# Kernel optimization log

Hardware: AMD Instinct MI355X
Metric: run time of the kernel (lower is better)

The kernel has to match this reference:

```python
import jax, jax.numpy as jnp
import numpy as np
import math

H = 768      # hidden_size
NH = 12      # num_head
DH = H // NH # head dim
FF = 4 * H
EPS = 1e-6

def _layernorm(x, g, b):
    mu = jnp.mean(x, axis=-1, keepdims=True)
    var = jnp.mean(jnp.square(x - mu), axis=-1, keepdims=True)
    return (x - mu) * jax.lax.rsqrt(var + EPS) * g + b

def setup_inputs() -> dict:
    key = jax.random.key(0)
    ks = jax.random.split(key, 16)
    B, N = 8, 1024
    xav = lambda k, i, o: jax.random.uniform(k, (i, o), jnp.float32, -1.0, 1.0) * math.sqrt(6.0 / (i + o))
    bias = lambda k, o: jax.random.normal(k, (o,), jnp.float32) * 1e-6
    return {
        "x": jax.random.normal(ks[0], (B, N, H), jnp.float32),
        "wq": xav(ks[1], H, H), "bq": bias(ks[2], H),
        "wk": xav(ks[3], H, H), "bk": bias(ks[4], H),
        "wv": xav(ks[5], H, H), "bv": bias(ks[6], H),
        "wo": xav(ks[7], H, H), "bo": bias(ks[8], H),
        "w1": xav(ks[9], H, FF), "b1": bias(ks[10], FF),
        "w2": xav(ks[11], FF, H), "b2": bias(ks[12], H),
        "g1": jnp.ones((H,), jnp.float32), "be1": jnp.zeros((H,), jnp.float32),
        "g2": jnp.ones((H,), jnp.float32), "be2": jnp.zeros((H,), jnp.float32),
    }

def reference(x, wq, bq, wk, bk, wv, bv, wo, bo, w1, b1, w2, b2, g1, be1, g2, be2):
    B, N, _ = x.shape
    x1 = _layernorm(x, g1, be1)
    # QKV projections -> (B, NH, N, DH)
    split = lambda t: t.reshape(B, N, NH, DH).transpose(0, 2, 1, 3)
    q = split(x1 @ wq + bq)
    k = split(x1 @ wk + bk)
    v = split(x1 @ wv + bv)
    # NOTE: original divides by sqrt(attention_size)=sqrt(H), not sqrt(DH)
    scores = jnp.einsum("bhqd,bhkd->bhqk", q, k) / math.sqrt(H)
    weights = jax.nn.softmax(scores, axis=-1)
    ctx = jnp.einsum("bhqk,bhkd->bhqd", weights, v)
    ctx = ctx.transpose(0, 2, 1, 3).reshape(B, N, H)
    attn_out = ctx @ wo + bo  # dropout is identity in eval
    x = x + attn_out
    x2 = _layernorm(x, g2, be2)
    h = jax.nn.gelu(x2 @ w1 + b1, approximate=False)  # torch F.gelu is exact erf gelu
    mlp_out = h @ w2 + b2
    x = x + mlp_out
    return (x, weights)
```

## Files before the change

kernel.cpp:

```cpp
#include <hip/hip_runtime.h>
#include <cstdint>
#include <cstddef>

#define H 768
#define NHEAD 12
#define DH 64
#define FFD 3072
#define BATCH 8
#define SEQ 1024
#define NTOK (BATCH*SEQ)
#define QKVS 2304

typedef __bf16 bf16x8 __attribute__((ext_vector_type(8)));
typedef float  floatx4 __attribute__((ext_vector_type(4)));

#define MFMA_BF16(a,b,c) __builtin_amdgcn_mfma_f32_16x16x32_bf16((a),(b),(c),0,0,0)

__device__ __forceinline__ void gload16(const void* g, void* l) {
    __builtin_amdgcn_global_load_lds((const __attribute__((address_space(1))) void*)g,
                                     (__attribute__((address_space(3))) void*)l,
                                     16, 0, 0);
}

__device__ __forceinline__ float gelu_erf(float x) {
    float z = fabsf(x) * 0.70710678118654752f;
    float t = __builtin_amdgcn_rcpf(1.0f + 0.3275911f * z);
    float poly = t * (0.254829592f +
               t * (-0.284496736f +
               t * (1.421413741f +
               t * (-1.453152027f +
               t * 1.061405429f))));
    float e = __expf(-z * z);
    float erfv = 1.0f - poly * e;
    erfv = copysignf(erfv, x);
    return 0.5f * x * (1.0f + erfv);
}

__global__ __launch_bounds__(256) void prep_kernel(
    const float* __restrict__ wq, const float* __restrict__ wk,
    const float* __restrict__ wv, const float* __restrict__ wo,
    const float* __restrict__ w1, const float* __restrict__ w2,
    const float* __restrict__ bq, const float* __restrict__ bk,
    const float* __restrict__ bv,
    __bf16* __restrict__ wqkvT, __bf16* __restrict__ woT,
    __bf16* __restrict__ w1T, __bf16* __restrict__ w2T,
    float* __restrict__ bqkv,
    const float* __restrict__ x, const float* __restrict__ g1,
    const float* __restrict__ be1, __bf16* __restrict__ x1b) {
    __shared__ float tile[32][33];
    int bid = blockIdx.x;
    int tid = threadIdx.x;
    if (bid < 6912) {
        const float* W; __bf16* T; int Kd, Nn, bx, by;
        if (bid < 1728) {
            int part = bid / 576;
            int rem = bid - part * 576;
            W = part == 0 ? wq : (part == 1 ? wk : wv);
            T = wqkvT + (size_t)part * H * H;
            Kd = H; Nn = H; bx = rem % 24; by = rem / 24;
        } else if (bid < 2304) {
            int rem = bid - 1728;
            W = wo; T = woT; Kd = H; Nn = H; bx = rem % 24; by = rem / 24;
        } else if (bid < 4608) {
            int rem = bid - 2304;
            W = w1; T = w1T; Kd = H; Nn = FFD; bx = rem % 96; by = rem / 96;
        } else {
            int rem = bid - 4608;
            W = w2; T = w2T; Kd = FFD; Nn = H; bx = rem % 24; by = rem / 24;
        }
        int tx = tid & 31, ty = tid >> 5;
        int n0 = bx * 32, k0 = by * 32;
#pragma unroll
        for (int i = 0; i < 32; i += 8)
            tile[ty + i][tx] = W[(size_t)(k0 + ty + i) * Nn + n0 + tx];
        __syncthreads();
#pragma unroll
        for (int i = 0; i < 32; i += 8)
            T[(size_t)(n0 + ty + i) * Kd + k0 + tx] = (__bf16)tile[tx][ty + i];
    } else if (bid < 6921) {
        int i = (bid - 6912) * 256 + tid;
        float v = i < H ? bq[i] : (i < 2 * H ? bk[i - H] : bv[i - 2 * H]);
        bqkv[i] = v;
    } else {
        int row  = (bid - 6921) * 4 + (tid >> 6);
        int lane = tid & 63;
        const float* xr = x + (size_t)row * H;
        float v[12];
        float s = 0.f;
#pragma unroll
        for (int i = 0; i < 12; i++) { v[i] = xr[lane + i * 64]; s += v[i]; }
#pragma unroll
        for (int m = 32; m >= 1; m >>= 1) s += __shfl_xor(s, m, 64);
        float mu = s * (1.0f / H);
        float q = 0.f;
#pragma unroll
        for (int i = 0; i < 12; i++) { float d = v[i] - mu; q += d * d; }
#pragma unroll
        for (int m = 32; m >= 1; m >>= 1) q += __shfl_xor(q, m, 64);
        float rstd = rsqrtf(q * (1.0f / H) + 1e-6f);
        __bf16* orow = x1b + (size_t)row * H;
#pragma unroll
        for (int i = 0; i < 12; i++) {
            int c = lane + i * 64;
            orow[c] = (__bf16)((v[i] - mu) * rstd * g1[c] + be1[c]);
        }
    }
}

__global__ __launch_bounds__(256) void ln_kernel(const float* __restrict__ x,
                                                 const float* __restrict__ g,
                                                 const float* __restrict__ be,
                                                 __bf16* __restrict__ out) {
    int row  = blockIdx.x * 4 + (threadIdx.x >> 6);
    int lane = threadIdx.x & 63;
    const float* xr = x + (size_t)row * H;
    float v[12];
    float s = 0.f;
#pragma unroll
    for (int i = 0; i < 12; i++) { v[i] = xr[lane + i * 64]; s += v[i]; }
#pragma unroll
    for (int m = 32; m >= 1; m >>= 1) s += __shfl_xor(s, m, 64);
    float mu = s * (1.0f / H);
    float q = 0.f;
#pragma unroll
    for (int i = 0; i < 12; i++) { float d = v[i] - mu; q += d * d; }
#pragma unroll
    for (int m = 32; m >= 1; m >>= 1) q += __shfl_xor(q, m, 64);
    float rstd = rsqrtf(q * (1.0f / H) + 1e-6f);
    __bf16* orow = out + (size_t)row * H;
#pragma unroll
    for (int i = 0; i < 12; i++) {
        int c = lane + i * 64;
        orow[c] = (__bf16)((v[i] - mu) * rstd * g[c] + be[c]);
    }
}

__global__ __launch_bounds__(256) void vtrans_kernel(const __bf16* __restrict__ qkv,
                                                     __bf16* __restrict__ vT) {
    __shared__ __bf16 tile[64][65];
    int b = blockIdx.z, h = blockIdx.y, n0 = blockIdx.x * 64;
    int tx = threadIdx.x, ty = threadIdx.y;
#pragma unroll
    for (int r = ty; r < 64; r += 4)
        tile[r][tx] = qkv[((size_t)b * SEQ + n0 + r) * QKVS + 2 * H + h * DH + tx];
    __syncthreads();
#pragma unroll
    for (int c = ty; c < 64; c += 4)
        vT[(((size_t)b * NHEAD + h) * DH + c) * SEQ + n0 + tx] = tile[tx][c];
}

template<bool GELU, bool HAS_RES, bool OUT_BF16>
__global__ __launch_bounds__(256) void gemm_kernel(const __bf16* __restrict__ A,
                                                   const __bf16* __restrict__ Bt,
                                                   const float* __restrict__ bias,
                                                   const float* __restrict__ res,
                                                   __bf16* __restrict__ obf,
                                                   float* __restrict__ ofp,
                                                   int Nn, int K) {
    __shared__ __bf16 As[128 * 64];
    __shared__ __bf16 Bs[128 * 64];
    int tid = threadIdx.x;
    int wave = tid >> 6, lane = tid & 63;
    int wr = wave >> 1, wc = wave & 1;
    int l15 = lane & 15, quad = lane >> 4;

    floatx4 acc[4][4];
    floatx4 zero = {0.f, 0.f, 0.f, 0.f};
#pragma unroll
    for (int i = 0; i < 4; i++)
#pragma unroll
        for (int j = 0; j < 4; j++) acc[i][j] = zero;

    int lrow = lane >> 3;
    int lcol = ((lane & 7) ^ lrow) * 8;
    const __bf16* Agc[4];
    const __bf16* Bgc[4];
    __bf16* AsDc[4];
    __bf16* BsDc[4];
#pragma unroll
    for (int cc = 0; cc < 4; cc++) {
        int chunk = wave * 4 + cc;
        int row = chunk * 8 + lrow;
        Agc[cc] = A + (size_t)(blockIdx.y * 128 + row) * K + lcol;
        Bgc[cc] = Bt + (size_t)(blockIdx.x * 128 + row) * K + lcol;
        AsDc[cc] = &As[chunk * 512];
        BsDc[cc] = &Bs[chunk * 512];
    }

    for (int k0 = 0; k0 < K; k0 += 64) {
#pragma unroll
        for (int cc = 0; cc < 4; cc++) {
            gload16(Agc[cc] + k0, AsDc[cc]);
            gload16(Bgc[cc] + k0, BsDc[cc]);
        }
        __syncthreads();
#pragma unroll
        for (int kk = 0; kk < 2; kk++) {
            int c16 = (kk * 4 + quad) ^ (l15 & 7);
            bf16x8 af[4], bfv[4];
#pragma unroll
            for (int i = 0; i < 4; i++)
                af[i] = *(const bf16x8*)&As[(wr * 64 + i * 16 + l15) * 64 + c16 * 8];
#pragma unroll
            for (int j = 0; j < 4; j++)
                bfv[j] = *(const bf16x8*)&Bs[(wc * 64 + j * 16 + l15) * 64 + c16 * 8];
#pragma unroll
            for (int i = 0; i < 4; i++)
#pragma unroll
                for (int j = 0; j < 4; j++)
                    acc[i][j] = MFMA_BF16(af[i], bfv[j], acc[i][j]);
        }
        __syncthreads();
    }

#pragma unroll
    for (int i = 0; i < 4; i++) {
        int row = blockIdx.y * 128 + wr * 64 + i * 16 + quad * 4;
#pragma unroll
        for (int j = 0; j < 4; j++) {
            int col = blockIdx.x * 128 + wc * 64 + j * 16 + l15;
            float bsv = bias[col];
#pragma unroll
            for (int r = 0; r < 4; r++) {
                float vv = acc[i][j][r] + bsv;
                if (GELU) vv = gelu_erf(vv);
                if (HAS_RES) vv += res[(size_t)(row + r) * Nn + col];
                if (OUT_BF16) obf[(size_t)(row + r) * Nn + col] = (__bf16)vv;
                else          ofp[(size_t)(row + r) * Nn + col] = vv;
            }
        }
    }
}

__device__ __forceinline__ int sbidx(int row, int col) {
    return row * 1024 + (col ^ ((row & 7) << 3));
}

__global__ __launch_bounds__(256, 4) void attn_kernel(const __bf16* __restrict__ qkv,
                                                      const __bf16* __restrict__ vT,
                                                      float* __restrict__ Wout,
                                                      __bf16* __restrict__ ctx) {
    __shared__ __bf16 Sb[16 * 1024];
    __shared__ __align__(16) float red[2][16][4];
    int tid = threadIdx.x;
    int wave = tid >> 6, lane = tid & 63, l15 = lane & 15, quad = lane >> 4;

    int linear = blockIdx.x + 64 * (blockIdx.y + 12 * blockIdx.z);
    int xcd = linear & 7;
    int j   = linear >> 3;
    int bh  = xcd + 8 * (j >> 6);
    int rt  = j & 63;
    int h = bh % NHEAD, b = bh / NHEAD;

    const size_t tokbase = (size_t)b * SEQ * QKVS + h * DH;
    const float scale = 0.03608439182435161f;

    const __bf16* qrow = qkv + tokbase + (size_t)(rt * 16 + l15) * QKVS;
    bf16x8 qf0 = *(const bf16x8*)(qrow + quad * 8);
    bf16x8 qf1 = *(const bf16x8*)(qrow + 32 + quad * 8);

    floatx4 s[16];
    const __bf16* kbase = qkv + tokbase + H;
#pragma unroll
    for (int i = 0; i < 16; i++) {
        int ct = wave * 16 + i;
        const __bf16* krow = kbase + (size_t)(ct * 16 + l15) * QKVS;
        bf16x8 kf0 = *(const bf16x8*)(krow + quad * 8);
        bf16x8 kf1 = *(const bf16x8*)(krow + 32 + quad * 8);
        floatx4 a = {0.f, 0.f, 0.f, 0.f};
        a = MFMA_BF16(qf0, kf0, a);
        a = MFMA_BF16(qf1, kf1, a);
#pragma unroll
        for (int r = 0; r < 4; r++) s[i][r] = a[r] * scale;
    }

    float m4[4];
#pragma unroll
    for (int r = 0; r < 4; r++) {
        float m = s[0][r];
#pragma unroll
        for (int i = 1; i < 16; i++) m = fmaxf(m, s[i][r]);
#pragma unroll
        for (int msk = 8; msk >= 1; msk >>= 1) m = fmaxf(m, __shfl_xor(m, msk, 64));
        m4[r] = m;
    }
    if (l15 == 0) {
#pragma unroll
        for (int r = 0; r < 4; r++) red[0][quad * 4 + r][wave] = m4[r];
    }
    __syncthreads();
    float mrow[4];
#pragma unroll
    for (int r = 0; r < 4; r++) {
        float4 rr = *(const float4*)&red[0][quad * 4 + r][0];
        mrow[r] = fmaxf(fmaxf(rr.x, rr.y), fmaxf(rr.z, rr.w));
    }

    float s4[4] = {0.f, 0.f, 0.f, 0.f};
#pragma unroll
    for (int i = 0; i < 16; i++) {
#pragma unroll
        for (int r = 0; r < 4; r++) {
            float e = __expf(s[i][r] - mrow[r]);
            s[i][r] = e;
            s4[r] += e;
        }
    }
#pragma unroll
    for (int r = 0; r < 4; r++) {
#pragma unroll
        for (int msk = 8; msk >= 1; msk >>= 1) s4[r] += __shfl_xor(s4[r], msk, 64);
    }
    if (l15 == 0) {
#pragma unroll
        for (int r = 0; r < 4; r++) red[1][quad * 4 + r][wave] = s4[r];
    }
    __syncthreads();
    float inv[4];
#pragma unroll
    for (int r = 0; r < 4; r++) {
        float4 rr = *(const float4*)&red[1][quad * 4 + r][0];
        inv[r] = 1.0f / (rr.x + rr.y + rr.z + rr.w);
    }

    size_t wbase = (((size_t)b * NHEAD + h) * SEQ + rt * 16) * SEQ;
#pragma unroll
    for (int i = 0; i < 16; i++) {
        int col = (wave * 16 + i) * 16 + l15;
#pragma unroll
        for (int r = 0; r < 4; r++) {
            float w = s[i][r] * inv[r];
            int row = quad * 4 + r;
            __builtin_nontemporal_store(w, &Wout[wbase + (size_t)row * SEQ + col]);
            Sb[sbidx(row, col)] = (__bf16)w;
        }
    }
    __syncthreads();

    floatx4 acc = {0.f, 0.f, 0.f, 0.f};
    const __bf16* vbase = vT + (((size_t)b * NHEAD + h) * DH + wave * 16 + l15) * SEQ;
#pragma unroll
    for (int c = 0; c < 32; c++) {
        int k0 = c * 32 + quad * 8;
        bf16x8 af = *(const bf16x8*)&Sb[sbidx(l15, k0)];
        bf16x8 bv = *(const bf16x8*)(vbase + k0);
        acc = MFMA_BF16(af, bv, acc);
    }
#pragma unroll
    for (int r = 0; r < 4; r++)
        ctx[((size_t)b * SEQ + rt * 16 + quad * 4 + r) * H + h * DH + wave * 16 + l15] =
            (__bf16)acc[r];
}

extern "C" void kernel_launch(void* const* d_in, const int* in_sizes, int n_in,
                              void* d_out, int out_size, void* d_ws, size_t ws_size,
                              hipStream_t stream) {
    const float* x   = (const float*)d_in[0];
    const float* wq  = (const float*)d_in[1];
    const float* bq  = (const float*)d_in[2];
    const float* wk  = (const float*)d_in[3];
    const float* bk  = (const float*)d_in[4];
    const float* wv  = (const float*)d_in[5];
    const float* bv  = (const float*)d_in[6];
    const float* wo  = (const float*)d_in[7];
    const float* bo  = (const float*)d_in[8];
    const float* w1  = (const float*)d_in[9];
    const float* b1  = (const float*)d_in[10];
    const float* w2  = (const float*)d_in[11];
    const float* b2  = (const float*)d_in[12];
    const float* g1  = (const float*)d_in[13];
    const float* be1 = (const float*)d_in[14];
    const float* g2  = (const float*)d_in[15];
    const float* be2 = (const float*)d_in[16];

    char* ws = (char*)d_ws;
    const size_t SZB = (size_t)NTOK * H * 2;
    __bf16* x1b  = (__bf16*)(ws);
    __bf16* qkvb = (__bf16*)(ws + SZB);
    __bf16* vTb  = (__bf16*)(ws + 4 * SZB);
    __bf16* ctxb = (__bf16*)(ws + 5 * SZB);
    __bf16* x2b  = (__bf16*)(ws + 6 * SZB);
    __bf16* hb   = (__bf16*)(ws + 7 * SZB);
    size_t off = 7 * SZB + (size_t)NTOK * FFD * 2;
    float* xattn = (float*)(ws + off); off += (size_t)NTOK * H * 4;
    __bf16* wqkvT = (__bf16*)(ws + off); off += (size_t)3 * H * H * 2;
    __bf16* woT  = (__bf16*)(ws + off); off += (size_t)H * H * 2;
    __bf16* w1T  = (__bf16*)(ws + off); off += (size_t)H * FFD * 2;
    __bf16* w2T  = (__bf16*)(ws + off); off += (size_t)FFD * H * 2;
    float* bqkv  = (float*)(ws + off); off += (size_t)3 * H * 4;

    float* outx = (float*)d_out;
    float* outw = (float*)d_out + (size_t)NTOK * H;

    prep_kernel<<<8969, 256, 0, stream>>>(wq, wk, wv, wo, w1, w2, bq, bk, bv,
                                          wqkvT, woT, w1T, w2T, bqkv,
                                          x, g1, be1, x1b);

    gemm_kernel<false, false, true><<<dim3(QKVS / 128, NTOK / 128), 256, 0, stream>>>(
        x1b, wqkvT, bqkv, nullptr, qkvb, nullptr, QKVS, H);

    vtrans_kernel<<<dim3(16, NHEAD, BATCH), dim3(64, 4), 0, stream>>>(qkvb, vTb);

    attn_kernel<<<dim3(64, NHEAD, BATCH), 256, 0, stream>>>(qkvb, vTb, outw, ctxb);

    gemm_kernel<false, true, false><<<dim3(H / 128, NTOK / 128), 256, 0, stream>>>(
        ctxb, woT, bo, x, nullptr, xattn, H, H);

    ln_kernel<<<NTOK / 4, 256, 0, stream>>>(xattn, g2, be2, x2b);

    gemm_kernel<true, false, true><<<dim3(FFD / 128, NTOK / 128), 256, 0, stream>>>(
        x2b, w1T, b1, nullptr, hb, nullptr, FFD, H);

    gemm_kernel<false, true, false><<<dim3(H / 128, NTOK / 128), 256, 0, stream>>>(
        hb, w2T, b2, xattn, nullptr, outx, H, FFD);
}
```

Measured before the change: 825.3 us.

## Fuse V transpose into QKV GEMM epilogue and use 64-row tiles for narrow GEMMs

```diff
diff --git a/kernel.cpp b/kernel.cpp
--- a/kernel.cpp
+++ b/kernel.cpp
@@ -135,79 +135,73 @@
     }
 }
 
-__global__ __launch_bounds__(256) void vtrans_kernel(const __bf16* __restrict__ qkv,
-                                                     __bf16* __restrict__ vT) {
-    __shared__ __bf16 tile[64][65];
-    int b = blockIdx.z, h = blockIdx.y, n0 = blockIdx.x * 64;
-    int tx = threadIdx.x, ty = threadIdx.y;
-#pragma unroll
-    for (int r = ty; r < 64; r += 4)
-        tile[r][tx] = qkv[((size_t)b * SEQ + n0 + r) * QKVS + 2 * H + h * DH + tx];
-    __syncthreads();
-#pragma unroll
-    for (int c = ty; c < 64; c += 4)
-        vT[(((size_t)b * NHEAD + h) * DH + c) * SEQ + n0 + tx] = tile[tx][c];
-}
-
-template<bool GELU, bool HAS_RES, bool OUT_BF16>
+template<bool GELU, bool HAS_RES, bool OUT_BF16, int TM, bool VWRITE, bool NT>
 __global__ __launch_bounds__(256) void gemm_kernel(const __bf16* __restrict__ A,
                                                    const __bf16* __restrict__ Bt,
                                                    const float* __restrict__ bias,
                                                    const float* __restrict__ res,
                                                    __bf16* __restrict__ obf,
                                                    float* __restrict__ ofp,
+                                                   __bf16* __restrict__ vT,
                                                    int Nn, int K) {
-    __shared__ __bf16 As[128 * 64];
+    __shared__ __bf16 As[TM * 64];
     __shared__ __bf16 Bs[128 * 64];
     int tid = threadIdx.x;
     int wave = tid >> 6, lane = tid & 63;
-    int wr = wave >> 1, wc = wave & 1;
     int l15 = lane & 15, quad = lane >> 4;
-
-    floatx4 acc[4][4];
+    constexpr int NJ = (TM == 128) ? 4 : 2;
+    int brow0 = (TM == 128) ? (wave >> 1) * 64 : 0;
+    int bcol0 = (TM == 128) ? (wave & 1) * 64 : wave * 32;
+
+    floatx4 acc[4][NJ];
     floatx4 zero = {0.f, 0.f, 0.f, 0.f};
 #pragma unroll
     for (int i = 0; i < 4; i++)
 #pragma unroll
-        for (int j = 0; j < 4; j++) acc[i][j] = zero;
+        for (int j = 0; j < NJ; j++) acc[i][j] = zero;
 
     int lrow = lane >> 3;
     int lcol = ((lane & 7) ^ lrow) * 8;
-    const __bf16* Agc[4];
+    constexpr int ACH = TM / 32;
+    const __bf16* Agc[ACH];
     const __bf16* Bgc[4];
-    __bf16* AsDc[4];
+    __bf16* AsDc[ACH];
     __bf16* BsDc[4];
+#pragma unroll
+    for (int cc = 0; cc < ACH; cc++) {
+        int chunk = wave * ACH + cc;
+        int row = chunk * 8 + lrow;
+        Agc[cc] = A + (size_t)(blockIdx.y * TM + row) * K + lcol;
+        AsDc[cc] = &As[chunk * 512];
+    }
 #pragma unroll
     for (int cc = 0; cc < 4; cc++) {
         int chunk = wave * 4 + cc;
         int row = chunk * 8 + lrow;
-        Agc[cc] = A + (size_t)(blockIdx.y * 128 + row) * K + lcol;
         Bgc[cc] = Bt + (size_t)(blockIdx.x * 128 + row) * K + lcol;
-        AsDc[cc] = &As[chunk * 512];
         BsDc[cc] = &Bs[chunk * 512];
     }
 
     for (int k0 = 0; k0 < K; k0 += 64) {
 #pragma unroll
-        for (int cc = 0; cc < 4; cc++) {
-            gload16(Agc[cc] + k0, AsDc[cc]);
-            gload16(Bgc[cc] + k0, BsDc[cc]);
-        }
+        for (int cc = 0; cc < ACH; cc++) gload16(Agc[cc] + k0, AsDc[cc]);
+#pragma unroll
+        for (int cc = 0; cc < 4; cc++)   gload16(Bgc[cc] + k0, BsDc[cc]);
         __syncthreads();
 #pragma unroll
         for (int kk = 0; kk < 2; kk++) {
             int c16 = (kk * 4 + quad) ^ (l15 & 7);
-            bf16x8 af[4], bfv[4];
+            bf16x8 af[4], bfv[NJ];
 #pragma unroll
             for (int i = 0; i < 4; i++)
-                af[i] = *(const bf16x8*)&As[(wr * 64 + i * 16 + l15) * 64 + c16 * 8];
-#pragma unroll
-            for (int j = 0; j < 4; j++)
-                bfv[j] = *(const bf16x8*)&Bs[(wc * 64 + j * 16 + l15) * 64 + c16 * 8];
+                af[i] = *(const bf16x8*)&As[(brow0 + i * 16 + l15) * 64 + c16 * 8];
+#pragma unroll
+            for (int j = 0; j < NJ; j++)
+                bfv[j] = *(const bf16x8*)&Bs[(bcol0 + j * 16 + l15) * 64 + c16 * 8];
 #pragma unroll
             for (int i = 0; i < 4; i++)
 #pragma unroll
-                for (int j = 0; j < 4; j++)
+                for (int j = 0; j < NJ; j++)
                     acc[i][j] = MFMA_BF16(af[i], bfv[j], acc[i][j]);
         }
         __syncthreads();
@@ -215,18 +209,29 @@
 
 #pragma unroll
     for (int i = 0; i < 4; i++) {
-        int row = blockIdx.y * 128 + wr * 64 + i * 16 + quad * 4;
-#pragma unroll
-        for (int j = 0; j < 4; j++) {
-            int col = blockIdx.x * 128 + wc * 64 + j * 16 + l15;
+        int row = blockIdx.y * TM + brow0 + i * 16 + quad * 4;
+#pragma unroll
+        for (int j = 0; j < NJ; j++) {
+            int col = blockIdx.x * 128 + bcol0 + j * 16 + l15;
             float bsv = bias[col];
 #pragma unroll
             for (int r = 0; r < 4; r++) {
                 float vv = acc[i][j][r] + bsv;
                 if (GELU) vv = gelu_erf(vv);
                 if (HAS_RES) vv += res[(size_t)(row + r) * Nn + col];
-                if (OUT_BF16) obf[(size_t)(row + r) * Nn + col] = (__bf16)vv;
-                else          ofp[(size_t)(row + r) * Nn + col] = vv;
+                if (VWRITE && blockIdx.x >= 12) {
+                    int vcol = col - 2 * H;
+                    int hh = vcol >> 6, dd = vcol & 63;
+                    int rr = row + r;
+                    int bb = rr >> 10, nn = rr & 1023;
+                    vT[(((size_t)bb * NHEAD + hh) * DH + dd) * SEQ + nn] = (__bf16)vv;
+                } else if (OUT_BF16) {
+                    obf[(size_t)(row + r) * Nn + col] = (__bf16)vv;
+                } else if (NT) {
+                    __builtin_nontemporal_store(vv, &ofp[(size_t)(row + r) * Nn + col]);
+                } else {
+                    ofp[(size_t)(row + r) * Nn + col] = vv;
+                }
             }
         }
     }
@@ -396,21 +401,23 @@
                                           wqkvT, woT, w1T, w2T, bqkv,
                                           x, g1, be1, x1b);
 
-    gemm_kernel<false, false, true><<<dim3(QKVS / 128, NTOK / 128), 256, 0, stream>>>(
-        x1b, wqkvT, bqkv, nullptr, qkvb, nullptr, QKVS, H);
-
-    vtrans_kernel<<<dim3(16, NHEAD, BATCH), dim3(64, 4), 0, stream>>>(qkvb, vTb);
+    gemm_kernel<false, false, true, 128, true, false>
+        <<<dim3(QKVS / 128, NTOK / 128), 256, 0, stream>>>(
+        x1b, wqkvT, bqkv, nullptr, qkvb, nullptr, vTb, QKVS, H);
 
     attn_kernel<<<dim3(64, NHEAD, BATCH), 256, 0, stream>>>(qkvb, vTb, outw, ctxb);
 
-    gemm_kernel<false, true, false><<<dim3(H / 128, NTOK / 128), 256, 0, stream>>>(
-        ctxb, woT, bo, x, nullptr, xattn, H, H);
+    gemm_kernel<false, true, false, 64, false, false>
+        <<<dim3(H / 128, NTOK / 64), 256, 0, stream>>>(
+        ctxb, woT, bo, x, nullptr, xattn, nullptr, H, H);
 
     ln_kernel<<<NTOK / 4, 256, 0, stream>>>(xattn, g2, be2, x2b);
 
-    gemm_kernel<true, false, true><<<dim3(FFD / 128, NTOK / 128), 256, 0, stream>>>(
-        x2b, w1T, b1, nullptr, hb, nullptr, FFD, H);
-
-    gemm_kernel<false, true, false><<<dim3(H / 128, NTOK / 128), 256, 0, stream>>>(
-        hb, w2T, b2, xattn, nullptr, outx, H, FFD);
-}
+    gemm_kernel<true, false, true, 128, false, false>
+        <<<dim3(FFD / 128, NTOK / 128), 256, 0, stream>>>(
+        x2b, w1T, b1, nullptr, hb, nullptr, nullptr, FFD, H);
+
+    gemm_kernel<false, true, false, 64, false, true>
+        <<<dim3(H / 128, NTOK / 64), 256, 0, stream>>>(
+        hb, w2T, b2, xattn, nullptr, outx, nullptr, H, FFD);
+}
```

After: 815.9 us. Within noise of the previous version (-1.1%).
